# Kernel tuning notes

Hardware: AMD Instinct MI355X
Metric: run time of the kernel (lower is better)

## Reference

```python
import jax, jax.numpy as jnp
import numpy as np
from jax.scipy.linalg import expm

N, T, IN, C, M = 64, 2048, 8, 2, 10  # batch, time, input_size, channels, hidden_size


def setup_inputs() -> dict:
    key = jax.random.key(0)
    k1, k2 = jax.random.split(key)
    x = jax.random.normal(k1, (N, T, IN), dtype=jnp.float32)
    # Lie-algebra generator parameters; small init keeps expm well-conditioned
    A = jax.random.normal(k2, (C, IN, M, M), dtype=jnp.float32) * (1.0 / (M * IN))
    return {"x": x, "A": A}


def dyadic_prod(X):
    # X: (N, T, C, m, m) -> cumulative (ordered) matrix product over time: (N, C, m, m)
    n, t, c, m, _ = X.shape
    levels = int(np.ceil(np.log2(t)))
    I = jnp.broadcast_to(jnp.eye(m, dtype=X.dtype), (n, 1, c, m, m))
    for _ in range(levels):
        if X.shape[1] % 2 == 1:
            X = jnp.concatenate([X, I], axis=1)  # pad with identity
        Xp = X.reshape(n, -1, 2, c, m, m)
        X = jnp.einsum('ntcij,ntcjk->ntcik', Xp[:, :, 0], Xp[:, :, 1])
    return X[:, 0]


def reference(x, A):
    # Skew-symmetrize generators -> so(m) Lie algebra elements, per channel/input dim
    skew = A - jnp.swapaxes(A, -1, -2)          # (C, IN, m, m)
    dX = x[:, 1:] - x[:, :-1]                   # (N, T-1, IN) path increments
    G = jnp.einsum('nti,cijk->ntcjk', dX, skew) # (N, T-1, C, m, m)
    Mexp = expm(G)                              # batched matrix exponential -> SO(m)
    return dyadic_prod(Mexp)                    # (N, C, m, m)
```

## Files before the change

kernel.cpp:

```cpp
#include <hip/hip_runtime.h>

#define NB     64
#define TT     2048
#define INQ    8
#define CC     2
#define MM     10
#define ROWP   12
#define MATS   124
#define SKST   12
#define BLK    512
#define SEGS   96
#define SLEN   11
#define NCHK   2
#define NCHAIN (NB*CC)

typedef float v2f __attribute__((ext_vector_type(2)));

__device__ __forceinline__ constexpr int triIdx(int k, int j) {
    return k * 10 + j - ((k + 1) * (k + 2)) / 2;
}

__device__ __forceinline__ float bperm_f(int addr_bytes, float v) {
    return __int_as_float(__builtin_amdgcn_ds_bpermute(addr_bytes, __float_as_int(v)));
}

__device__ __forceinline__ void trow_pk(const float* __restrict__ Tri,
                                        v2f* A, v2f* R, const v2f* S, float cj) {
    v2f t[MM];
    t[0] = -S[1] * Tri[triIdx(0, 1)];
    #pragma unroll
    for (int j = 1; j < MM; ++j) t[j] = S[0] * Tri[triIdx(0, j)];
    #pragma unroll
    for (int k = 1; k < MM; ++k) {
        const v2f a = S[k];
        #pragma unroll
        for (int j = 0; j < MM; ++j) {
            if (k == j) continue;
            if (j == 0 && k == 1) continue;
            if (j > k) t[j] += a * Tri[triIdx(k, j)];
            else       t[j] -= a * Tri[triIdx(j, k)];
        }
    }
    #pragma unroll
    for (int j = 0; j < MM; ++j) { A[j] = t[j]; R[j] += cj * t[j]; }
}

__device__ __forceinline__ void pair_combine(float* buf_s, int ls, int rs, int pq) {
    float lrow[5][MM];
    #pragma unroll
    for (int r = 0; r < 5; ++r) {
        const float4* lr = reinterpret_cast<const float4*>(
            &buf_s[ls * MATS + (pq * 5 + r) * ROWP]);
        const float4 a = lr[0], b = lr[1], c4 = lr[2];
        lrow[r][0] = a.x;  lrow[r][1] = a.y;  lrow[r][2] = a.z;  lrow[r][3] = a.w;
        lrow[r][4] = b.x;  lrow[r][5] = b.y;  lrow[r][6] = b.z;  lrow[r][7] = b.w;
        lrow[r][8] = c4.x; lrow[r][9] = c4.y;
    }
    float d[5][MM];
    #pragma unroll
    for (int r = 0; r < 5; ++r)
        #pragma unroll
        for (int j = 0; j < MM; ++j)
            d[r][j] = 0.0f;
    #pragma unroll
    for (int k = 0; k < MM; ++k) {
        const float4* rr = reinterpret_cast<const float4*>(&buf_s[rs * MATS + k * ROWP]);
        const float4 a = rr[0], b = rr[1], c4 = rr[2];
        float rrow[MM];
        rrow[0] = a.x;  rrow[1] = a.y;  rrow[2] = a.z;  rrow[3] = a.w;
        rrow[4] = b.x;  rrow[5] = b.y;  rrow[6] = b.z;  rrow[7] = b.w;
        rrow[8] = c4.x; rrow[9] = c4.y;
        #pragma unroll
        for (int r = 0; r < 5; ++r) {
            const float lv = lrow[r][k];
            #pragma unroll
            for (int j = 0; j < MM; ++j)
                d[r][j] += lv * rrow[j];
        }
    }
    float* dst = &buf_s[ls * MATS + pq * 5 * ROWP];
    #pragma unroll
    for (int r = 0; r < 5; ++r) {
        float4* drow = reinterpret_cast<float4*>(dst + r * ROWP);
        drow[0] = make_float4(d[r][0], d[r][1], d[r][2], d[r][3]);
        drow[1] = make_float4(d[r][4], d[r][5], d[r][6], d[r][7]);
        drow[2] = make_float4(d[r][8], d[r][9], 0.0f, 0.0f);
    }
}

__global__ __launch_bounds__(BLK, 1)
void dev_serial(const float* __restrict__ x,
                const float* __restrict__ A,
                float* __restrict__ ws)
{
    __shared__ __align__(16) float skq_s[45 * SKST];
    __shared__ __align__(16) float buf_s[SEGS * MATS];

    const int tid   = threadIdx.x;
    const int chain = blockIdx.x >> 1;
    const int qt    = blockIdx.x & 1;
    const int n     = chain >> 1;
    const int c     = chain & 1;

    if (tid < 45 * 8) {
        const int e  = tid >> 3;
        const int ip = tid & 7;
        int k = 0, r2 = e;
        while (r2 >= 9 - k) { r2 -= (9 - k); ++k; }
        const int j = k + 1 + r2;
        const float* Ab = A + (size_t)(c * INQ + ip) * (MM * MM);
        skq_s[e * SKST + ip] = Ab[k * MM + j] - Ab[j * MM + k];
    }
    __syncthreads();

    const int wv  = tid >> 6;
    const int wl  = tid & 63;
    const int g   = wl / 5;
    const int r   = wl - 5 * g;
    const bool act = (wl < 60);
    const int seg = wv * 12 + g;
    const int p0  = 2 * r;

    v2f R01[MM];
    #pragma unroll
    for (int j = 0; j < MM; ++j)
        R01[j] = (v2f){ (j == p0) ? 1.0f : 0.0f, (j == p0 + 1) ? 1.0f : 0.0f };

    const float4* px = reinterpret_cast<const float4*>(x + (size_t)n * TT * INQ);
    const int t0 = qt * (SEGS * SLEN) + seg * SLEN;

    #pragma unroll 1
    for (int s = 0; s < SLEN; ++s) {
        const int t = t0 + s;
        const int tc = (t     > TT - 1) ? TT - 1 : t;
        const int t1 = (t + 1 > TT - 1) ? TT - 1 : t + 1;
        const float4 a0 = px[2 * tc], a1 = px[2 * tc + 1];
        const float4 b0 = px[2 * t1], b1 = px[2 * t1 + 1];
        float dx[INQ];
        dx[0] = b0.x - a0.x; dx[1] = b0.y - a0.y;
        dx[2] = b0.z - a0.z; dx[3] = b0.w - a0.w;
        dx[4] = b1.x - a1.x; dx[5] = b1.y - a1.y;
        dx[6] = b1.z - a1.z; dx[7] = b1.w - a1.w;

        float tvv[9];
        {
            const float* srow = &skq_s[(9 * r) * SKST];
            #pragma unroll
            for (int i = 0; i < 9; ++i) {
                const float4 s0 = *reinterpret_cast<const float4*>(srow + i * SKST);
                const float4 s1 = *reinterpret_cast<const float4*>(srow + i * SKST + 4);
                tvv[i] = dx[0] * s0.x + dx[1] * s0.y + dx[2] * s0.z + dx[3] * s0.w
                       + dx[4] * s1.x + dx[5] * s1.y + dx[6] * s1.z + dx[7] * s1.w;
            }
        }

        float Tri[45];
        const int base = (wl - r) * 4;
        #pragma unroll
        for (int e = 0; e < 45; ++e)
            Tri[e] = bperm_f(base + (e / 9) * 4, tvv[e % 9]);

        __builtin_amdgcn_s_setprio(1);
        v2f A01[MM];
        trow_pk(Tri, A01, R01, R01, 1.0f);
        trow_pk(Tri, A01, R01, A01, 0.5f);
        trow_pk(Tri, A01, R01, A01, 0.16666667f);
        trow_pk(Tri, A01, R01, A01, 0.041666668f);
        trow_pk(Tri, A01, R01, A01, 0.0083333338f);
        __builtin_amdgcn_s_setprio(0);
    }

    if (act) {
        float* dst = &buf_s[seg * MATS];
        float4* d0 = reinterpret_cast<float4*>(dst + p0 * ROWP);
        d0[0] = make_float4(R01[0].x, R01[1].x, R01[2].x, R01[3].x);
        d0[1] = make_float4(R01[4].x, R01[5].x, R01[6].x, R01[7].x);
        d0[2] = make_float4(R01[8].x, R01[9].x, 0.0f, 0.0f);
        float4* d1 = reinterpret_cast<float4*>(dst + (p0 + 1) * ROWP);
        d1[0] = make_float4(R01[0].y, R01[1].y, R01[2].y, R01[3].y);
        d1[1] = make_float4(R01[4].y, R01[5].y, R01[6].y, R01[7].y);
        d1[2] = make_float4(R01[8].y, R01[9].y, 0.0f, 0.0f);
    }
    __syncthreads();

    #pragma unroll 1
    for (int span = 2; span <= 32; span <<= 1) {
        const int np = SEGS / span;
        if (tid < 2 * np) {
            const int pr = tid >> 1;
            const int pq = tid & 1;
            pair_combine(buf_s, pr * span, pr * span + (span >> 1), pq);
        }
        __syncthreads();
    }
    if (tid < 2) pair_combine(buf_s, 0, 32, tid);
    __syncthreads();
    if (tid < 2) pair_combine(buf_s, 0, 64, tid);
    __syncthreads();

    if (tid < 30) {
        const float4 v = reinterpret_cast<const float4*>(buf_s)[tid];
        reinterpret_cast<float4*>(ws)[((size_t)chain * NCHK + qt) * 30 + tid] = v;
    }
}

__global__ __launch_bounds__(256)
void dev_tree2(const float* __restrict__ ws, float* __restrict__ out)
{
    __shared__ __align__(16) float buf_s[2 * MATS];
    const int tid   = threadIdx.x;
    const int chain = blockIdx.x;

    if (tid < 60) {
        const int m  = tid / 30;
        const int o4 = tid - m * 30;
        const float4 v = reinterpret_cast<const float4*>(ws)[((size_t)chain * 2 + m) * 30 + o4];
        reinterpret_cast<float4*>(&buf_s[m * MATS])[o4] = v;
    }
    __syncthreads();

    if (tid < 2)
        pair_combine(buf_s, 0, 1, tid);
    __syncthreads();

    if (tid < 100) {
        const int i = tid / 10;
        const int j = tid - i * 10;
        out[(size_t)chain * 100 + tid] = buf_s[i * ROWP + j];
    }
}

extern "C" void kernel_launch(void* const* d_in, const int* in_sizes, int n_in,
                              void* d_out, int out_size, void* d_ws, size_t ws_size,
                              hipStream_t stream) {
    (void)in_sizes; (void)n_in; (void)out_size; (void)ws_size;
    const float* x = (const float*)d_in[0];
    const float* A = (const float*)d_in[1];
    float* out = (float*)d_out;
    float* ws  = (float*)d_ws;

    dev_serial<<<dim3(NCHAIN * NCHK), dim3(BLK), 0, stream>>>(x, A, ws);
    dev_tree2<<<dim3(NCHAIN), dim3(256), 0, stream>>>(ws, out);
}
```

Measured before the change: 97.31 us.

## Fuse final tree combine via last-block atomic and share Tri through LDS scratch

Replaces the 45 per-step ds_bpermute cross-lane shuffles with each lane writing its 9 generator values into a per-segment LDS scratch and reading back all 45 with vector loads. Removes the second kernel launch. The last block of each chain to finish, detected with an atomic counter, now does the final pair combine and writes the output. This adds a memset of the flag array on the stream each call, plus agent-scope atomic stores and loads for the cross-block handoff.

Measured after the change: 96.67 us. Within noise of the previous version (-0.7%).

```diff
diff --git a/kernel.cpp b/kernel.cpp
--- a/kernel.cpp
+++ b/kernel.cpp
@@ -13,15 +13,13 @@
 #define SLEN   11
 #define NCHK   2
 #define NCHAIN (NB*CC)
+#define SCRS   60
+#define FLAGS_OFF_F (NCHAIN * NCHK * 120)
 
 typedef float v2f __attribute__((ext_vector_type(2)));
 
 __device__ __forceinline__ constexpr int triIdx(int k, int j) {
     return k * 10 + j - ((k + 1) * (k + 2)) / 2;
-}
-
-__device__ __forceinline__ float bperm_f(int addr_bytes, float v) {
-    return __int_as_float(__builtin_amdgcn_ds_bpermute(addr_bytes, __float_as_int(v)));
 }
 
 __device__ __forceinline__ void trow_pk(const float* __restrict__ Tri,
@@ -43,6 +41,17 @@
     }
     #pragma unroll
     for (int j = 0; j < MM; ++j) { A[j] = t[j]; R[j] += cj * t[j]; }
+}
+
+__device__ __forceinline__ void taylor5(const float* __restrict__ Tri, v2f* R01) {
+    __builtin_amdgcn_s_setprio(1);
+    v2f A01[MM];
+    trow_pk(Tri, A01, R01, R01, 1.0f);
+    trow_pk(Tri, A01, R01, A01, 0.5f);
+    trow_pk(Tri, A01, R01, A01, 0.16666667f);
+    trow_pk(Tri, A01, R01, A01, 0.041666668f);
+    trow_pk(Tri, A01, R01, A01, 0.0083333338f);
+    __builtin_amdgcn_s_setprio(0);
 }
 
 __device__ __forceinline__ void pair_combine(float* buf_s, int ls, int rs, int pq) {
@@ -91,10 +100,12 @@
 __global__ __launch_bounds__(BLK, 1)
 void dev_serial(const float* __restrict__ x,
                 const float* __restrict__ A,
-                float* __restrict__ ws)
+                float* __restrict__ ws,
+                float* __restrict__ out)
 {
     __shared__ __align__(16) float skq_s[45 * SKST];
     __shared__ __align__(16) float buf_s[SEGS * MATS];
+    __shared__ int won_s;
 
     const int tid   = threadIdx.x;
     const int chain = blockIdx.x >> 1;
@@ -121,6 +132,9 @@
     const int seg = wv * 12 + g;
     const int p0  = 2 * r;
 
+    float* scr  = &buf_s[seg * SCRS];
+    float* scrw = act ? scr : &buf_s[96 * SCRS];
+
     v2f R01[MM];
     #pragma unroll
     for (int j = 0; j < MM; ++j)
@@ -128,6 +142,7 @@
 
     const float4* px = reinterpret_cast<const float4*>(x + (size_t)n * TT * INQ);
     const int t0 = qt * (SEGS * SLEN) + seg * SLEN;
+    const float* srow = &skq_s[(9 * r) * SKST];
 
     #pragma unroll 1
     for (int s = 0; s < SLEN; ++s) {
@@ -143,32 +158,35 @@
         dx[6] = b1.z - a1.z; dx[7] = b1.w - a1.w;
 
         float tvv[9];
-        {
-            const float* srow = &skq_s[(9 * r) * SKST];
-            #pragma unroll
-            for (int i = 0; i < 9; ++i) {
-                const float4 s0 = *reinterpret_cast<const float4*>(srow + i * SKST);
-                const float4 s1 = *reinterpret_cast<const float4*>(srow + i * SKST + 4);
-                tvv[i] = dx[0] * s0.x + dx[1] * s0.y + dx[2] * s0.z + dx[3] * s0.w
-                       + dx[4] * s1.x + dx[5] * s1.y + dx[6] * s1.z + dx[7] * s1.w;
-            }
-        }
+        #pragma unroll
+        for (int i = 0; i < 9; ++i) {
+            const float4 s0 = *reinterpret_cast<const float4*>(srow + i * SKST);
+            const float4 s1 = *reinterpret_cast<const float4*>(srow + i * SKST + 4);
+            tvv[i] = dx[0] * s0.x + dx[1] * s0.y + dx[2] * s0.z + dx[3] * s0.w
+                   + dx[4] * s1.x + dx[5] * s1.y + dx[6] * s1.z + dx[7] * s1.w;
+        }
+
+        *reinterpret_cast<float4*>(scrw + 12 * r)     = make_float4(tvv[0], tvv[1], tvv[2], tvv[3]);
+        *reinterpret_cast<float4*>(scrw + 12 * r + 4) = make_float4(tvv[4], tvv[5], tvv[6], tvv[7]);
+        scrw[12 * r + 8] = tvv[8];
 
         float Tri[45];
-        const int base = (wl - r) * 4;
-        #pragma unroll
-        for (int e = 0; e < 45; ++e)
-            Tri[e] = bperm_f(base + (e / 9) * 4, tvv[e % 9]);
-
-        __builtin_amdgcn_s_setprio(1);
-        v2f A01[MM];
-        trow_pk(Tri, A01, R01, R01, 1.0f);
-        trow_pk(Tri, A01, R01, A01, 0.5f);
-        trow_pk(Tri, A01, R01, A01, 0.16666667f);
-        trow_pk(Tri, A01, R01, A01, 0.041666668f);
-        trow_pk(Tri, A01, R01, A01, 0.0083333338f);
-        __builtin_amdgcn_s_setprio(0);
-    }
+        #pragma unroll
+        for (int q2 = 0; q2 < 5; ++q2) {
+            const float4 u0 = *reinterpret_cast<const float4*>(scr + 12 * q2);
+            const float4 u1 = *reinterpret_cast<const float4*>(scr + 12 * q2 + 4);
+            const float  u2 = scr[12 * q2 + 8];
+            Tri[9 * q2 + 0] = u0.x; Tri[9 * q2 + 1] = u0.y;
+            Tri[9 * q2 + 2] = u0.z; Tri[9 * q2 + 3] = u0.w;
+            Tri[9 * q2 + 4] = u1.x; Tri[9 * q2 + 5] = u1.y;
+            Tri[9 * q2 + 6] = u1.z; Tri[9 * q2 + 7] = u1.w;
+            Tri[9 * q2 + 8] = u2;
+        }
+
+        taylor5(Tri, R01);
+    }
+
+    __syncthreads();
 
     if (act) {
         float* dst = &buf_s[seg * MATS];
@@ -198,31 +216,27 @@
     if (tid < 2) pair_combine(buf_s, 0, 64, tid);
     __syncthreads();
 
-    if (tid < 30) {
-        const float4 v = reinterpret_cast<const float4*>(buf_s)[tid];
-        reinterpret_cast<float4*>(ws)[((size_t)chain * NCHK + qt) * 30 + tid] = v;
-    }
-}
-
-__global__ __launch_bounds__(256)
-void dev_tree2(const float* __restrict__ ws, float* __restrict__ out)
-{
-    __shared__ __align__(16) float buf_s[2 * MATS];
-    const int tid   = threadIdx.x;
-    const int chain = blockIdx.x;
-
-    if (tid < 60) {
-        const int m  = tid / 30;
-        const int o4 = tid - m * 30;
-        const float4 v = reinterpret_cast<const float4*>(ws)[((size_t)chain * 2 + m) * 30 + o4];
-        reinterpret_cast<float4*>(&buf_s[m * MATS])[o4] = v;
-    }
-    __syncthreads();
-
-    if (tid < 2)
-        pair_combine(buf_s, 0, 1, tid);
-    __syncthreads();
-
+    if (tid < 120)
+        __hip_atomic_store(&ws[((size_t)chain * NCHK + qt) * 120 + tid], buf_s[tid],
+                           __ATOMIC_RELAXED, __HIP_MEMORY_SCOPE_AGENT);
+    __syncthreads();
+
+    int* flags = reinterpret_cast<int*>(ws + FLAGS_OFF_F);
+    if (tid == 0)
+        won_s = __hip_atomic_fetch_add(&flags[chain], 1,
+                                       __ATOMIC_ACQ_REL, __HIP_MEMORY_SCOPE_AGENT);
+    __syncthreads();
+    if (won_s == 0) return;
+
+    if (tid < 240) {
+        const int m = tid / 120, f = tid - m * 120;
+        buf_s[m * MATS + f] =
+            __hip_atomic_load(&ws[((size_t)chain * NCHK + m) * 120 + f],
+                              __ATOMIC_RELAXED, __HIP_MEMORY_SCOPE_AGENT);
+    }
+    __syncthreads();
+    if (tid < 2) pair_combine(buf_s, 0, 1, tid);
+    __syncthreads();
     if (tid < 100) {
         const int i = tid / 10;
         const int j = tid - i * 10;
@@ -239,6 +253,7 @@
     float* out = (float*)d_out;
     float* ws  = (float*)d_ws;
 
-    dev_serial<<<dim3(NCHAIN * NCHK), dim3(BLK), 0, stream>>>(x, A, ws);
-    dev_tree2<<<dim3(NCHAIN), dim3(256), 0, stream>>>(ws, out);
-}
+    hipMemsetAsync((char*)d_ws + FLAGS_OFF_F * sizeof(float), 0,
+                   NCHAIN * sizeof(int), stream);
+    dev_serial<<<dim3(NCHAIN * NCHK), dim3(BLK), 0, stream>>>(x, A, ws, out);
+}
```
